# Optimization experiments

Hardware: AMD Instinct MI355X
Metric: run time of the kernel (lower is better)

The kernel has to match this reference:

```python
import jax, jax.numpy as jnp
import numpy as np


def setup_inputs() -> dict:
    key = jax.random.key(0)
    ks = jax.random.split(key, 6)
    B, C_in, C_out, H, W = 4, 256, 128, 64, 64
    return {
        "p": jax.random.normal(ks[0], (B, C_in, H, W), dtype=jnp.float32),
        "b": jax.random.normal(ks[1], (B, C_in, H, W), dtype=jnp.float32),
        "Wq": jax.random.normal(ks[2], (C_out, C_in), dtype=jnp.float32) * 0.05,
        "bq": jax.random.normal(ks[3], (C_out,), dtype=jnp.float32) * 0.05,
        "Wk": jax.random.normal(ks[4], (C_out, C_in), dtype=jnp.float32) * 0.05,
        "bk": jax.random.normal(ks[5], (C_out,), dtype=jnp.float32) * 0.05,
    }


def reference(p, b, Wq, bq, Wk, bk):
    # p, b: [B, C, H, W]; 1x1 convs are per-pixel GEMMs over channels.
    B, C, H, W = p.shape
    N = H * W
    p_flat = p.reshape(B, C, N)  # [B, C, N]
    b_flat = b.reshape(B, C, N)  # [B, C, N]
    # query = Conv1x1(p) -> [B, O, N] -> permuted to [B, N, O]
    q = jnp.einsum("bcn,oc->bno", p_flat, Wq) + bq  # [B, N, O]
    # key = Conv1x1(b) -> [B, O, N]
    k = jnp.einsum("bcn,oc->bon", b_flat, Wk) + bk[:, None]  # [B, O, N]
    energy = jnp.einsum("bno,bom->bnm", q, k)  # [B, N, N]
    attention = jax.nn.softmax(energy, axis=-1)
    # value = b flattened, attention applied over spatial tokens
    out = jnp.einsum("bnm,bcm->bcn", attention, b_flat)  # [B, C, N]
    return out.reshape(B, C, H, W)
```

## Files before the change

kernel.cpp:

```cpp
#include <hip/hip_runtime.h>
#include <stdint.h>


#define B_ 4
#define C_ 256
#define O_ 128
#define N_ 4096

#define AP 72
#define PP 40

typedef float v4f __attribute__((ext_vector_type(4)));
typedef short v8s __attribute__((ext_vector_type(8)));
typedef _Float16 v8h __attribute__((ext_vector_type(8)));
typedef uint32_t u32;
typedef unsigned short u16;

__device__ __forceinline__ u16 bf16_rne(float f) {
  u32 u = __builtin_bit_cast(u32, f);
  u += 0x7fffu + ((u >> 16) & 1u);
  return (u16)(u >> 16);
}
__device__ __forceinline__ float bf16_f(u16 s) {
  u32 u = ((u32)s) << 16;
  return __builtin_bit_cast(float, u);
}
__device__ __forceinline__ u16 f16_rne(float f) {
  _Float16 h = (_Float16)f;
  return __builtin_bit_cast(u16, h);
}
__device__ __forceinline__ float f16_f(u16 s) {
  return (float)__builtin_bit_cast(_Float16, s);
}
__device__ __forceinline__ v4f mfma16(v8s a, v8s b, v4f c) {
  return __builtin_amdgcn_mfma_f32_16x16x32_bf16(a, b, c, 0, 0, 0);
}
__device__ __forceinline__ v4f mfma16h(v8h a, v8h b, v4f c) {
  return __builtin_amdgcn_mfma_f32_16x16x32_f16(a, b, c, 0, 0, 0);
}
__device__ __forceinline__ void gl16(const u16* g, u16* l) {
  __builtin_amdgcn_global_load_lds(
      (const __attribute__((address_space(1))) u32*)g,
      (__attribute__((address_space(3))) u32*)l, 16, 0, 0);
}
template <int CTRL>
__device__ __forceinline__ float dppadd(float x) {
  int yi = __builtin_amdgcn_update_dpp(0, __builtin_bit_cast(int, x), CTRL,
                                       0xf, 0xf, true);
  return x + __builtin_bit_cast(float, yi);
}
__device__ __forceinline__ float sum16(float x) {
  x = dppadd<0xB1>(x);
  x = dppadd<0x4E>(x);
  x = dppadd<0x141>(x);
  x = dppadd<0x140>(x);
  return x;
}

__global__ __launch_bounds__(256) void k_proj(
    const float* __restrict__ Xp, const float* __restrict__ Wq,
    const float* __restrict__ bq, const float* __restrict__ Xb,
    const float* __restrict__ Wk, const float* __restrict__ bk,
    u16* __restrict__ Qh, u16* __restrict__ Kh, u16* __restrict__ Vbf) {
  __shared__ __align__(16) short ah[64 * AP];
  __shared__ __align__(16) short al[64 * AP];
  __shared__ __align__(16) short wh[128 * AP];
  __shared__ __align__(16) short wl[128 * AP];
  const int tid = threadIdx.x;
  const int inst = blockIdx.x >> 8;
  const float* X = inst ? Xb : Xp;
  const float* W = inst ? Wk : Wq;
  const float* bias = inst ? bk : bq;
  const int b = (blockIdx.x >> 6) & 3;
  const int n0 = (blockIdx.x & 63) << 6;
  const int w = tid >> 6, lane = tid & 63, l15 = lane & 15, quad = lane >> 4;
  v4f acc[8];
#pragma unroll
  for (int t = 0; t < 8; t++) acc[t] = (v4f){0.f, 0.f, 0.f, 0.f};

  for (int c0 = 0; c0 < C_; c0 += 64) {
    __syncthreads();
    {
      const int c = tid >> 2, nch = (tid & 3) << 4;
      const float* s = X + ((size_t)(b * C_ + c0 + c)) * N_ + n0 + nch;
      float4 f0 = ((const float4*)s)[0], f1 = ((const float4*)s)[1],
             f2 = ((const float4*)s)[2], f3 = ((const float4*)s)[3];
      float v[16] = {f0.x, f0.y, f0.z, f0.w, f1.x, f1.y, f1.z, f1.w,
                     f2.x, f2.y, f2.z, f2.w, f3.x, f3.y, f3.z, f3.w};
      u16 hh[16];
#pragma unroll
      for (int j = 0; j < 16; j++) {
        u16 h = bf16_rne(v[j]);
        u16 l = bf16_rne(v[j] - bf16_f(h));
        hh[j] = h;
        ah[(nch + j) * AP + c] = (short)h;
        al[(nch + j) * AP + c] = (short)l;
      }
      if (inst) {
        u32 pk[8];
#pragma unroll
        for (int jj = 0; jj < 8; jj++)
          pk[jj] = (u32)hh[2 * jj] | ((u32)hh[2 * jj + 1] << 16);
        u16* vd = Vbf + ((size_t)(b * C_ + c0 + c)) * N_ + n0 + nch;
        ((uint4*)vd)[0] = make_uint4(pk[0], pk[1], pk[2], pk[3]);
        ((uint4*)vd)[1] = make_uint4(pk[4], pk[5], pk[6], pk[7]);
      }
    }
    {
      const int o = tid >> 1, cch = (tid & 1) << 5;
      const float* s = W + (size_t)o * C_ + c0 + cch;
#pragma unroll
      for (int jj = 0; jj < 8; jj++) {
        float4 f = ((const float4*)s)[jj];
        float v[4] = {f.x, f.y, f.z, f.w};
#pragma unroll
        for (int j = 0; j < 4; j++) {
          u16 h = bf16_rne(v[j]);
          u16 l = bf16_rne(v[j] - bf16_f(h));
          wh[o * AP + cch + jj * 4 + j] = (short)h;
          wl[o * AP + cch + jj * 4 + j] = (short)l;
        }
      }
    }
    __syncthreads();
#pragma unroll
    for (int s = 0; s < 2; s++) {
      v8s a_h = *(const v8s*)&ah[(16 * w + l15) * AP + 32 * s + 8 * quad];
      v8s a_l = *(const v8s*)&al[(16 * w + l15) * AP + 32 * s + 8 * quad];
#pragma unroll
      for (int to = 0; to < 8; to++) {
        v8s b_h = *(const v8s*)&wh[(16 * to + l15) * AP + 32 * s + 8 * quad];
        v8s b_l = *(const v8s*)&wl[(16 * to + l15) * AP + 32 * s + 8 * quad];
        acc[to] = mfma16(a_h, b_h, acc[to]);
        acc[to] = mfma16(a_h, b_l, acc[to]);
        acc[to] = mfma16(a_l, b_h, acc[to]);
      }
    }
  }
#pragma unroll
  for (int to = 0; to < 8; to++) {
    const int o = 16 * to + l15;
    const float bv = bias[o];
    u16* dst = inst ? Kh : Qh;
#pragma unroll
    for (int r = 0; r < 4; r++) {
      const int n = n0 + 16 * w + 4 * quad + r;
      float v = acc[to][r] + bv;
      const size_t idx = (size_t)(b * N_ + n) * O_ + o;
      dst[idx] = f16_rne(v);
    }
  }
}

__global__ __launch_bounds__(256, 2) void k_flash(
    const u16* __restrict__ Qh, const u16* __restrict__ Khp,
    const u16* __restrict__ Vbf, u16* __restrict__ Opart,
    float* __restrict__ lpart) {
  __shared__ __align__(16) short smem[27136];
  short* Pt = smem + 24576;

  const int tid = threadIdx.x;
  const int w = tid >> 6, lane = tid & 63, l15 = lane & 15, quad = lane >> 4;
  const int h = blockIdx.x & 1;
  const int qt = (blockIdx.x >> 1) & 63;
  const int b = blockIdx.x >> 7;
  const int n0 = qt << 6;
  const int tok0 = h << 11;

  const u16* khb = Khp + (size_t)b * N_ * O_;
  const u16* vb = Vbf + (size_t)b * C_ * N_;

  v8h qh[4];
  {
    const u16* qrh = Qh + (size_t)(b * N_ + n0 + 16 * w + l15) * O_;
#pragma unroll
    for (int s = 0; s < 4; s++) {
      qh[s] = *(const v8h*)(qrh + 32 * s + 8 * quad);
    }
  }

  v4f oacc[16];
#pragma unroll
  for (int t = 0; t < 16; t++) oacc[t] = (v4f){0.f, 0.f, 0.f, 0.f};
  float lstate[4] = {0.f, 0.f, 0.f, 0.f};

  auto stage = [&](int mtn, int bi) {
    const int m0n = tok0 + (mtn << 5);
    short* kd = smem + bi * 12288;
    short* vd = kd + 4096;
#pragma unroll
    for (int i = 0; i < 2; i++) {
      const int R = 8 * w + 4 * i;
      const int rl = R + (lane >> 4);
      const int cg = (lane & 15) ^ (rl & 15);
      gl16(khb + ((size_t)(m0n + rl) << 7) + (cg << 3), (u16*)(kd + (R << 7)));
    }
#pragma unroll
    for (int i = 0; i < 4; i++) {
      const int R = 64 * w + 16 * i;
      const int rl = R + (lane >> 2);
      const int cg = (lane & 3) ^ ((rl >> 1) & 3);
      gl16(vb + (size_t)rl * N_ + m0n + (cg << 3), (u16*)(vd + (R << 5)));
    }
  };

  stage(0, 0);

#pragma unroll 1
  for (int mt = 0; mt < 64; mt++) {
    const int pr = mt & 1;
    __syncthreads();
    if (mt + 1 < 64) stage(mt + 1, 1 - pr);
    const short* kc = smem + pr * 12288;
    const short* vc = kc + 4096;

    v4f eh[2];
#pragma unroll
    for (int t = 0; t < 2; t++) {
      eh[t] = (v4f){0.f, 0.f, 0.f, 0.f};
    }
#pragma unroll
    for (int s = 0; s < 4; s++) {
#pragma unroll
      for (int t = 0; t < 2; t++) {
        const int off = ((16 * t + l15) << 7) + (((4 * s + quad) ^ l15) << 3);
        const v8h kf = *(const v8h*)&kc[off];
        eh[t] = mfma16h(qh[s], kf, eh[t]);
      }
    }

#pragma unroll
    for (int r = 0; r < 4; r++) {
      float p0 = __expf(eh[0][r]);
      float p1 = __expf(eh[1][r]);
      lstate[r] += sum16(p0 + p1);
      Pt[(16 * w + 4 * quad + r) * PP + l15] = (short)bf16_rne(p0);
      Pt[(16 * w + 4 * quad + r) * PP + 16 + l15] = (short)bf16_rne(p1);
    }
    __builtin_amdgcn_s_waitcnt(0xC07F);
    asm volatile("s_barrier" ::: "memory");

    v8s af[4];
#pragma unroll
    for (int rw = 0; rw < 4; rw++)
      af[rw] = *(const v8s*)&Pt[(16 * rw + l15) * PP + 8 * quad];
#pragma unroll
    for (int cg = 0; cg < 4; cg++) {
      const int ch = 64 * w + 16 * cg + l15;
      const int voff = (ch << 5) + ((quad ^ ((ch >> 1) & 3)) << 3);
      const v8s vf = *(const v8s*)&vc[voff];
#pragma unroll
      for (int rw = 0; rw < 4; rw++)
        oacc[rw * 4 + cg] = mfma16(af[rw], vf, oacc[rw * 4 + cg]);
    }
  }

  __syncthreads();
  u16* outx = (u16*)smem;
#pragma unroll
  for (int rw = 0; rw < 4; rw++)
#pragma unroll
    for (int cg = 0; cg < 4; cg++) {
      const int ch = 64 * w + 16 * cg + l15;
      const v4f o = oacc[rw * 4 + cg];
      u32* q = (u32*)outx;
      const int base = ch * 36 + 8 * rw + 2 * quad;
      q[base] = (u32)bf16_rne(o[0]) | ((u32)bf16_rne(o[1]) << 16);
      q[base + 1] = (u32)bf16_rne(o[2]) | ((u32)bf16_rne(o[3]) << 16);
    }
  if (l15 == 0) {
#pragma unroll
    for (int r = 0; r < 4; r++)
      lpart[(size_t)blockIdx.x * 64 + 16 * w + 4 * quad + r] = lstate[r];
  }
  __syncthreads();
  {
    u16* od = Opart + (size_t)blockIdx.x * 16384;
    const int cr = tid >> 2, nch = (tid & 3) << 4;
#pragma unroll
    for (int it = 0; it < 4; it++) {
      const int c = cr + 64 * it;
      const u16* srcr = &outx[c * 72 + nch];
      uint4* dst = (uint4*)(od + c * 64 + nch);
      dst[0] = ((const uint4*)srcr)[0];
      dst[1] = ((const uint4*)srcr)[1];
    }
  }
}

__global__ __launch_bounds__(256) void k_merge(const u16* __restrict__ Opart,
                                               const float* __restrict__ lpart,
                                               float* __restrict__ out) {
  const int idx = blockIdx.x * 256 + threadIdx.x;
  const int e4 = idx << 2;
  const int b = e4 >> 20;
  const int c = (e4 >> 12) & 255;
  const int n = e4 & 4095;
  const int qt = n >> 6, row = n & 63;
  const int g = (b * 64 + qt) * 2;
  const u16* q0 = Opart + (size_t)g * 16384 + c * 64 + row;
  ushort4 a0 = *(const ushort4*)q0;
  ushort4 a1 = *(const ushort4*)(q0 + 16384);
  float4 l0 = *(const float4*)(lpart + (size_t)g * 64 + row);
  float4 l1 = *(const float4*)(lpart + (size_t)g * 64 + 64 + row);
  float4 o;
  o.x = (bf16_f(a0.x) + bf16_f(a1.x)) / (l0.x + l1.x);
  o.y = (bf16_f(a0.y) + bf16_f(a1.y)) / (l0.y + l1.y);
  o.z = (bf16_f(a0.z) + bf16_f(a1.z)) / (l0.z + l1.z);
  o.w = (bf16_f(a0.w) + bf16_f(a1.w)) / (l0.w + l1.w);
  *(float4*)(out + e4) = o;
}

extern "C" void kernel_launch(void* const* d_in, const int* in_sizes, int n_in,
                              void* d_out, int out_size, void* d_ws, size_t ws_size,
                              hipStream_t stream) {
  const float* p = (const float*)d_in[0];
  const float* bb = (const float*)d_in[1];
  const float* Wq = (const float*)d_in[2];
  const float* bq = (const float*)d_in[3];
  const float* Wk = (const float*)d_in[4];
  const float* bk = (const float*)d_in[5];
  float* out = (float*)d_out;

  const size_t plane = (size_t)B_ * N_ * O_;
  u16* Qh = (u16*)d_ws;
  u16* Kh = Qh + plane;
  u16* Vbf = Kh + plane;
  u16* Opart = Vbf + 2 * plane;
  float* lpart = (float*)(Opart + (size_t)512 * 16384);

  hipLaunchKernelGGL(k_proj, dim3(512), dim3(256), 0, stream, p, Wq, bq, bb,
                     Wk, bk, Qh, Kh, Vbf);
  hipLaunchKernelGGL(k_flash, dim3(B_ * 64 * 2), dim3(256), 0, stream, Qh, Kh,
                     Vbf, Opart, lpart);
  hipLaunchKernelGGL(k_merge, dim3((B_ * C_ * N_) / (256 * 4)), dim3(256), 0,
                     stream, Opart, lpart, out);
}
```

Before: 177.5 us.

## Load V fragments straight to registers, remap blocks per XCD, swizzle P tile

V tiles are now read from global memory directly into per-lane MFMA B-fragment registers, no longer staged through LDS, which cuts LDS use from about 54KB to 36KB and removes one set of async copies per step. Block indices are remapped so that each XCD gets a fixed (batch, half) pair, with the output slot recomputed explicitly, to improve L2 reuse of K and V. The P scratch tile switches from a padded layout to an XOR-swizzled 64-wide layout to avoid bank conflicts. The row-sum reduction is moved after the PV MFMAs so it can overlap with them. The risk is that the direct V global loads expose more memory latency, since they are not double-buffered.

```diff
diff --git a/kernel.cpp b/kernel.cpp
--- a/kernel.cpp
+++ b/kernel.cpp
@@ -8,7 +8,6 @@
 #define N_ 4096
 
 #define AP 72
-#define PP 40
 
 typedef float v4f __attribute__((ext_vector_type(4)));
 typedef short v8s __attribute__((ext_vector_type(8)));
@@ -156,16 +155,17 @@
     const u16* __restrict__ Qh, const u16* __restrict__ Khp,
     const u16* __restrict__ Vbf, u16* __restrict__ Opart,
     float* __restrict__ lpart) {
-  __shared__ __align__(16) short smem[27136];
-  short* Pt = smem + 24576;
+  __shared__ __align__(16) short smem[18432];
+  short* const Pt = smem + 8192;
 
   const int tid = threadIdx.x;
   const int w = tid >> 6, lane = tid & 63, l15 = lane & 15, quad = lane >> 4;
-  const int h = blockIdx.x & 1;
-  const int qt = (blockIdx.x >> 1) & 63;
-  const int b = blockIdx.x >> 7;
+  const int xcd = blockIdx.x & 7;
+  const int b = xcd >> 1, h = xcd & 1;
+  const int qt = blockIdx.x >> 3;
   const int n0 = qt << 6;
   const int tok0 = h << 11;
+  const int og = (b << 7) + (qt << 1) + h;
 
   const u16* khb = Khp + (size_t)b * N_ * O_;
   const u16* vb = Vbf + (size_t)b * C_ * N_;
@@ -174,9 +174,7 @@
   {
     const u16* qrh = Qh + (size_t)(b * N_ + n0 + 16 * w + l15) * O_;
 #pragma unroll
-    for (int s = 0; s < 4; s++) {
-      qh[s] = *(const v8h*)(qrh + 32 * s + 8 * quad);
-    }
+    for (int s = 0; s < 4; s++) qh[s] = *(const v8h*)(qrh + 32 * s + 8 * quad);
   }
 
   v4f oacc[16];
@@ -186,8 +184,7 @@
 
   auto stage = [&](int mtn, int bi) {
     const int m0n = tok0 + (mtn << 5);
-    short* kd = smem + bi * 12288;
-    short* vd = kd + 4096;
+    short* kd = smem + bi * 4096;
 #pragma unroll
     for (int i = 0; i < 2; i++) {
       const int R = 8 * w + 4 * i;
@@ -195,13 +192,15 @@
       const int cg = (lane & 15) ^ (rl & 15);
       gl16(khb + ((size_t)(m0n + rl) << 7) + (cg << 3), (u16*)(kd + (R << 7)));
     }
-#pragma unroll
-    for (int i = 0; i < 4; i++) {
-      const int R = 64 * w + 16 * i;
-      const int rl = R + (lane >> 2);
-      const int cg = (lane & 3) ^ ((rl >> 1) & 3);
-      gl16(vb + (size_t)rl * N_ + m0n + (cg << 3), (u16*)(vd + (R << 5)));
-    }
+  };
+
+  v8s vfr[4];
+  const u16* vbase = vb + (size_t)(64 * w + l15) * N_ + (quad << 3);
+  auto loadV = [&](int mtn) {
+    const int m0 = tok0 + (mtn << 5);
+#pragma unroll
+    for (int cg = 0; cg < 4; cg++)
+      vfr[cg] = *(const v8s*)(vbase + (size_t)(cg << 4) * N_ + m0);
   };
 
   stage(0, 0);
@@ -210,15 +209,13 @@
   for (int mt = 0; mt < 64; mt++) {
     const int pr = mt & 1;
     __syncthreads();
+    loadV(mt);
     if (mt + 1 < 64) stage(mt + 1, 1 - pr);
-    const short* kc = smem + pr * 12288;
-    const short* vc = kc + 4096;
+    const short* kc = smem + pr * 4096;
 
     v4f eh[2];
 #pragma unroll
-    for (int t = 0; t < 2; t++) {
-      eh[t] = (v4f){0.f, 0.f, 0.f, 0.f};
-    }
+    for (int t = 0; t < 2; t++) eh[t] = (v4f){0.f, 0.f, 0.f, 0.f};
 #pragma unroll
     for (int s = 0; s < 4; s++) {
 #pragma unroll
@@ -229,30 +226,35 @@
       }
     }
 
+    float pp[4];
 #pragma unroll
     for (int r = 0; r < 4; r++) {
       float p0 = __expf(eh[0][r]);
       float p1 = __expf(eh[1][r]);
-      lstate[r] += sum16(p0 + p1);
-      Pt[(16 * w + 4 * quad + r) * PP + l15] = (short)bf16_rne(p0);
-      Pt[(16 * w + 4 * quad + r) * PP + 16 + l15] = (short)bf16_rne(p1);
+      const int row = 16 * w + 4 * quad + r;
+      const int sw = (row & 7) << 3;
+      Pt[(row << 6) + (l15 ^ sw)] = (short)bf16_rne(p0);
+      Pt[(row << 6) + ((16 + l15) ^ sw)] = (short)bf16_rne(p1);
+      pp[r] = p0 + p1;
     }
     __builtin_amdgcn_s_waitcnt(0xC07F);
     asm volatile("s_barrier" ::: "memory");
 
     v8s af[4];
 #pragma unroll
-    for (int rw = 0; rw < 4; rw++)
-      af[rw] = *(const v8s*)&Pt[(16 * rw + l15) * PP + 8 * quad];
-#pragma unroll
-    for (int cg = 0; cg < 4; cg++) {
-      const int ch = 64 * w + 16 * cg + l15;
-      const int voff = (ch << 5) + ((quad ^ ((ch >> 1) & 3)) << 3);
-      const v8s vf = *(const v8s*)&vc[voff];
+    for (int rw = 0; rw < 4; rw++) {
+      const int row = (rw << 4) + l15;
+      const int col = (quad << 3) ^ ((row & 7) << 3);
+      af[rw] = *(const v8s*)&Pt[(row << 6) + col];
+    }
+#pragma unroll
+    for (int cg = 0; cg < 4; cg++)
 #pragma unroll
       for (int rw = 0; rw < 4; rw++)
-        oacc[rw * 4 + cg] = mfma16(af[rw], vf, oacc[rw * 4 + cg]);
-    }
+        oacc[rw * 4 + cg] = mfma16(af[rw], vfr[cg], oacc[rw * 4 + cg]);
+
+#pragma unroll
+    for (int r = 0; r < 4; r++) lstate[r] += sum16(pp[r]);
   }
 
   __syncthreads();
@@ -271,11 +273,11 @@
   if (l15 == 0) {
 #pragma unroll
     for (int r = 0; r < 4; r++)
-      lpart[(size_t)blockIdx.x * 64 + 16 * w + 4 * quad + r] = lstate[r];
+      lpart[(size_t)og * 64 + 16 * w + 4 * quad + r] = lstate[r];
   }
   __syncthreads();
   {
-    u16* od = Opart + (size_t)blockIdx.x * 16384;
+    u16* od = Opart + (size_t)og * 16384;
     const int cr = tid >> 2, nch = (tid & 3) << 4;
 #pragma unroll
     for (int it = 0; it < 4; it++) {
```

After: 177.9 us. No clear change (+0.2%).
